# Optimization experiments

Hardware: AMD Instinct MI355X
Metric: run time of the kernel (lower is better)

## Reference

```python
import jax, jax.numpy as jnp
import numpy as np

BN_INV = 1.0 / np.float32(np.sqrt(1.0 + 1e-5))  # eval BN with running_mean=0, running_var=1


def _conv(x, w, stride):
    return jax.lax.conv_general_dilated(
        x, w, (stride, stride), [(1, 1), (1, 1)],
        dimension_numbers=('NCHW', 'OIHW', 'NCHW'))


def _se(x, w1, b1, w2, b2):
    # squeeze-excite: global avg pool -> fc -> relu -> fc -> sigmoid -> scale
    y = x.mean(axis=(2, 3))                       # (B, C)
    y = jax.nn.relu(y @ w1.T + b1)
    y = jax.nn.sigmoid(y @ w2.T + b2)
    return x * y[:, :, None, None]


def _squash(s):
    n2 = jnp.sum(s * s, axis=-1, keepdims=True)
    n = jnp.sqrt(n2)
    return s * (n2 / (1.0 + n2)) / (n + 1e-8)


def _block(x, cw, g, b, s1w, s1b, s2w, s2b, stride):
    h = _conv(x, cw, stride)
    h = h * (g * BN_INV)[None, :, None, None] + b[None, :, None, None]
    h = jax.nn.relu(h)
    return _se(h, s1w, s1b, s2w, s2b)


def setup_inputs() -> dict:
    key = jax.random.key(0)
    ks = jax.random.split(key, 32)
    rn = lambda i, shape, s=1.0: s * jax.random.normal(ks[i], shape, dtype=jnp.float32)
    d = {}
    d['x'] = rn(0, (64, 1, 128, 128))
    # feature extractor
    d['conv1_w'] = rn(1, (16, 1, 3, 3), 0.3)
    d['bn1_g'] = 1.0 + rn(2, (16,), 0.1)
    d['bn1_b'] = rn(3, (16,), 0.1)
    d['se1_w1'] = rn(4, (1, 16), 0.2); d['se1_b1'] = rn(5, (1,), 0.1)
    d['se1_w2'] = rn(6, (16, 1), 0.2); d['se1_b2'] = rn(7, (16,), 0.1)
    d['conv2_w'] = rn(8, (32, 16, 3, 3), 0.1)
    d['bn2_g'] = 1.0 + rn(9, (32,), 0.1)
    d['bn2_b'] = rn(10, (32,), 0.1)
    d['se2_w1'] = rn(11, (2, 32), 0.2); d['se2_b1'] = rn(12, (2,), 0.1)
    d['se2_w2'] = rn(13, (32, 2), 0.2); d['se2_b2'] = rn(14, (32,), 0.1)
    d['conv3_w'] = rn(15, (64, 32, 3, 3), 0.07)
    d['bn3_g'] = 1.0 + rn(16, (64,), 0.1)
    d['bn3_b'] = rn(17, (64,), 0.1)
    d['se3_w1'] = rn(18, (4, 64), 0.15); d['se3_b1'] = rn(19, (4,), 0.1)
    d['se3_w2'] = rn(20, (64, 4), 0.15); d['se3_b2'] = rn(21, (64,), 0.1)
    # primary capsules conv: 64 -> 8 caps * 8 dim = 64 channels, stride 2
    d['pc_w'] = rn(22, (64, 64, 3, 3), 0.05)
    d['pc_b'] = rn(23, (64,), 0.05)
    # digit capsule transform: (1, 2048, 3, 16, 8)
    d['W_digit'] = 0.01 * jax.random.normal(ks[24], (1, 2048, 3, 16, 8), dtype=jnp.float32)
    return d


def reference(x, conv1_w, bn1_g, bn1_b, se1_w1, se1_b1, se1_w2, se1_b2,
              conv2_w, bn2_g, bn2_b, se2_w1, se2_b1, se2_w2, se2_b2,
              conv3_w, bn3_g, bn3_b, se3_w1, se3_b1, se3_w2, se3_b2,
              pc_w, pc_b, W_digit):
    h = _block(x, conv1_w, bn1_g, bn1_b, se1_w1, se1_b1, se1_w2, se1_b2, 1)
    h = _block(h, conv2_w, bn2_g, bn2_b, se2_w1, se2_b1, se2_w2, se2_b2, 2)
    h = _block(h, conv3_w, bn3_g, bn3_b, se3_w1, se3_b1, se3_w2, se3_b2, 2)
    # primary capsules: conv -> (B, 8 caps, 8 dim, 16*16) -> (B, 2048, 8)
    u = _conv(h, pc_w, 2) + pc_b[None, :, None, None]     # (B, 64, 16, 16)
    B = u.shape[0]
    u = u.reshape(B, 8, 8, -1).transpose(0, 1, 3, 2).reshape(B, -1, 8)
    u = _squash(u)                                        # (B, 2048, 8)
    # u_hat[b,i,c,d] = sum_e W[0,i,c,d,e] * u[b,i,e]  (avoids torch's W.repeat)
    u_hat = jnp.einsum('icde,bie->bicd', W_digit[0], u)   # (B, 2048, 3, 16)
    b_ij = jnp.zeros((B, u_hat.shape[1], u_hat.shape[2], 1), u_hat.dtype)
    v_j = None
    for _ in range(3):  # fixed routing iterations
        c_ij = jax.nn.softmax(b_ij, axis=2)
        s_j = jnp.sum(c_ij * u_hat, axis=1, keepdims=True)  # (B,1,3,16)
        v_j = _squash(s_j)
        b_ij = b_ij + jnp.sum(u_hat * v_j, axis=-1, keepdims=True)
    v = v_j[:, 0]                                          # (B, 3, 16)
    return jnp.sqrt(jnp.sum(v * v, axis=-1))               # (B, 3) class lengths
```

## Files before the change

### kernel.cpp

```cpp
#include <hip/hip_runtime.h>
#include <math.h>

#define BN_INV_F 0.9999950000374997f

__device__ __forceinline__ void gload_lds4(const float* g, float* l) {
    __builtin_amdgcn_global_load_lds(
        (const __attribute__((address_space(1))) void*)g,
        (__attribute__((address_space(3))) void*)l, 4, 0, 0);
}
__device__ __forceinline__ void gload_lds16(const float* g, float* l) {
    __builtin_amdgcn_global_load_lds(
        (const __attribute__((address_space(1))) void*)g,
        (__attribute__((address_space(3))) void*)l, 16, 0, 0);
}

__global__ __launch_bounds__(256) void wtrans_all_k(
    const float* __restrict__ w1, const float* __restrict__ w2,
    const float* __restrict__ w3, const float* __restrict__ wp,
    float* __restrict__ w1t, float* __restrict__ w2t,
    float* __restrict__ w3t, float* __restrict__ wpt)
{
    int i = blockIdx.x * 256 + threadIdx.x;
    if (i < 144) {
        int co = i % 16, k = i / 16;
        w1t[i] = w1[co * 9 + k];
    } else if (i < 4752) {
        int t = i - 144;
        int co = t % 32, rk = t / 32, cin = rk / 9, k = rk % 9;
        w2t[t] = w2[(co * 16 + cin) * 9 + k];
    } else if (i < 23184) {
        int t = i - 4752;
        int co = t % 64, rk = t / 64, cin = rk / 9, k = rk % 9;
        w3t[t] = w3[(co * 32 + cin) * 9 + k];
    } else if (i < 60048) {
        int t = i - 23184;
        int co = t % 64, rk = t / 64, cin = rk / 9, k = rk % 9;
        wpt[t] = wp[(co * 64 + cin) * 9 + k];
    }
}

template <int CIN, int CINB, int COUT, int COB, int HIN, int HOUT, int STRIDE,
          int TW, int ROWS_T, int PPT, int CB, int NTHREADS,
          bool BN_RELU, bool SE_SUM, int HSE_IN, int KSPLIT>
__device__ __forceinline__ void conv_body(
    const float* __restrict__ in, const float* __restrict__ wt,
    const float* __restrict__ gamma, const float* __restrict__ beta,
    float* __restrict__ out, size_t pstride,
    float* __restrict__ se_sum, const float* __restrict__ se_sums_in,
    const float* __restrict__ se_w1, const float* __restrict__ se_b1,
    const float* __restrict__ se_w2, const float* __restrict__ se_b2,
    float inv_spatial)
{
    constexpr int WIN = HIN, WOUT = HOUT;
    constexpr int TH = ROWS_T * PPT;
    constexpr int IH_T = (TH - 1) * STRIDE + 3;
    constexpr int NW = NTHREADS / 64;
    constexpr int NCHUNK = CINB / CB;
    constexpr int SEGS = (WIN >= 64) ? (WIN / 64) : 1;
    constexpr int PAIRS = (IH_T + 1) / 2;
    constexpr int NG = COUT / COB;
    constexpr int IHW = IH_T * WIN;
    constexpr int CHUNK_BYTES = CB * IHW * 4;
    constexpr bool FAST16 = (CHUNK_BYTES % 1024) == 0;
    constexpr int NISS = CHUNK_BYTES / 1024;
    static_assert(NTHREADS == TW * ROWS_T, "geometry");
    static_assert(TW == WOUT, "tile must span full output width");
    static_assert(CINB % CB == 0, "chunking");
    static_assert(WIN % 64 == 0 || WIN == 32, "stage width");

    const int b = blockIdx.z;
    const int gy = blockIdx.y;
    const int ty = blockIdx.x;
    const int tid = threadIdx.x;
    const int wo = tid % TW;
    const int rg = tid / TW;
    const int g = gy % NG;
    const int kk = gy / NG;
    const int cin0 = kk * CINB;

    __shared__ float in_t[2][CB * IH_T * WIN];
    __shared__ float scl[CIN];
    __shared__ float gl[COB], bl[COB];
    __shared__ float red[NW][COB];
    __shared__ float hid[HSE_IN > 0 ? HSE_IN : 1];

    const float* inb = in + (size_t)b * CIN * HIN * WIN;
    const int gr0 = ty * TH * STRIDE - 1;
    const int wos = wo * STRIDE;
    const int wvid = tid >> 6, lane = tid & 63;
    const bool interior = (gr0 >= 0) && (gr0 + IH_T <= HIN);

    auto stage = [&](int c, int buf) {
        const int cb0 = cin0 + c * CB;
        float* bb = &in_t[buf][0];
        if (FAST16 && interior) {
            for (int i = wvid; i < NISS; i += NW) {
                int fe = i * 256 + lane * 4;
                int ci = fe / IHW;
                int rem = fe - ci * IHW;
                int lr = rem / WIN;
                int lc = rem - lr * WIN;
                const float* gsrc = inb + (size_t)(cb0 + ci) * (HIN * WIN)
                                  + (size_t)(gr0 + lr) * WIN + lc;
                gload_lds16(gsrc, bb + i * 256);
            }
        } else if (WIN >= 64) {
            for (int r = wvid; r < CB * IH_T; r += NW) {
                int ci = r / IH_T, lr = r - ci * IH_T;
                int gr = gr0 + lr;
                float* ldst = bb + (ci * IH_T + lr) * WIN;
                if (gr >= 0 && gr < HIN) {
                    const float* gsrc = inb + (size_t)(cb0 + ci) * HIN * WIN + (size_t)gr * WIN;
#pragma unroll
                    for (int s = 0; s < SEGS; ++s)
                        gload_lds4(gsrc + s * 64 + lane, ldst + s * 64);
                } else {
#pragma unroll
                    for (int s = 0; s < SEGS; ++s) ldst[s * 64 + lane] = 0.0f;
                }
            }
        } else {
            for (int pz = wvid; pz < CB * PAIRS; pz += NW) {
                int ci = pz / PAIRS, q = pz - ci * PAIRS;
                int lr0 = q * 2;
                int nr = (lr0 + 1 < IH_T) ? 2 : 1;
                int grr = gr0 + lr0;
                float* ldst = bb + (ci * IH_T + lr0) * WIN;
                if (nr == 2 && grr >= 0 && grr + 1 < HIN) {
                    const float* gsrc = inb + (size_t)(cb0 + ci) * HIN * WIN + (size_t)grr * WIN + lane;
                    gload_lds4(gsrc, ldst);
                } else {
                    for (int e = lane; e < nr * WIN; e += 64) {
                        int rr = e / WIN, cc = e - rr * WIN;
                        int gr = grr + rr;
                        ldst[e] = (gr >= 0 && gr < HIN)
                            ? inb[(size_t)(cb0 + ci) * HIN * WIN + (size_t)gr * WIN + cc] : 0.0f;
                    }
                }
            }
        }
    };

    stage(0, 0);

    if (HSE_IN > 0) {
        if (tid < HSE_IN) {
            float a = se_b1[tid];
            for (int c = 0; c < CIN; ++c)
                a = fmaf(se_sums_in[b * CIN + c] * inv_spatial, se_w1[tid * CIN + c], a);
            hid[tid] = fmaxf(a, 0.0f);
        }
        __syncthreads();
        if (tid < CIN) {
            float a = se_b2[tid];
            for (int h = 0; h < HSE_IN; ++h)
                a = fmaf(hid[h], se_w2[tid * HSE_IN + h], a);
            scl[tid] = 1.0f / (1.0f + expf(-a));
        }
    } else {
        for (int t = tid; t < CIN; t += NTHREADS) scl[t] = 1.0f;
    }
    if (tid < COB) {
        int co = g * COB + tid;
        if (BN_RELU) {
            gl[tid] = gamma[co] * BN_INV_F;
            bl[tid] = beta[co];
        } else {
            gl[tid] = (kk == 0) ? gamma[co] : 0.0f;
        }
    }

    float acc[PPT][COB];
#pragma unroll
    for (int p = 0; p < PPT; ++p)
#pragma unroll
        for (int co = 0; co < COB; ++co) acc[p][co] = 0.0f;

    int cur = 0;
    for (int c = 0; c < NCHUNK; ++c) {
        asm volatile("s_waitcnt vmcnt(0)" ::: "memory");
        __syncthreads();
        if (c + 1 < NCHUNK) stage(c + 1, cur ^ 1);

        const float* bb = &in_t[cur][0];
#pragma unroll
        for (int ci = 0; ci < CB; ++ci) {
            const int cw = cin0 + c * CB + ci;
            const float sc = scl[cw];
            const float* wtap = wt + (size_t)cw * 9 * COUT + g * COB;
            const float* bb_ci = bb + ci * IH_T * WIN;
#pragma unroll
            for (int kh = 0; kh < 3; ++kh) {
#pragma unroll
                for (int kw = 0; kw < 3; ++kw) {
                    const float* wrow = wtap + (kh * 3 + kw) * COUT;
#pragma unroll
                    for (int p = 0; p < PPT; ++p) {
                        const float* row = bb_ci + ((rg + p * ROWS_T) * STRIDE + kh) * WIN;
                        int wi = wos + kw - 1;
                        float v;
                        if (kw == 0) {
                            v = row[wi < 0 ? 0 : wi];
                            if (wi < 0) v = 0.0f;
                        } else if (STRIDE == 1 && kw == 2) {
                            v = row[wi >= WIN ? WIN - 1 : wi];
                            if (wi >= WIN) v = 0.0f;
                        } else {
                            v = row[wi];
                        }
                        v *= sc;
#pragma unroll
                        for (int co = 0; co < COB; ++co)
                            acc[p][co] = fmaf(wrow[co], v, acc[p][co]);
                    }
                }
            }
        }
        cur ^= 1;
    }

    float tsum[COB];
#pragma unroll
    for (int co = 0; co < COB; ++co) tsum[co] = 0.0f;
    float* ob = out + (size_t)kk * pstride
              + ((size_t)b * COUT + (size_t)g * COB) * HOUT * WOUT;
#pragma unroll
    for (int p = 0; p < PPT; ++p) {
        const int ho = ty * TH + rg + p * ROWS_T;
#pragma unroll
        for (int co = 0; co < COB; ++co) {
            float v;
            if (BN_RELU)
                v = fmaxf(fmaf(acc[p][co], gl[co], bl[co]), 0.0f);
            else
                v = acc[p][co] + gl[co];
            ob[(size_t)co * HOUT * WOUT + ho * WOUT + wo] = v;
            tsum[co] += v;
        }
    }

    if (SE_SUM) {
#pragma unroll
        for (int co = 0; co < COB; ++co) {
            float v = tsum[co];
            for (int off = 32; off; off >>= 1) v += __shfl_down(v, off, 64);
            if (lane == 0) red[wvid][co] = v;
        }
        __syncthreads();
        if (tid < COB) {
            float v = 0.0f;
#pragma unroll
            for (int k = 0; k < NW; ++k) v += red[k][tid];
            atomicAdd(&se_sum[b * COUT + g * COB + tid], v);
        }
    }
}

template <int CIN, int CINB, int COUT, int WCO, int HIN, int HOUT,
          int TW, int CB, int NTHREADS,
          bool BN_RELU, bool SE_SUM, int HSE_IN>
__device__ __forceinline__ void conv_ws2_body(
    const float* __restrict__ in, const float* __restrict__ wt,
    const float* __restrict__ gamma, const float* __restrict__ beta,
    float* __restrict__ out,
    float* __restrict__ se_sum, const float* __restrict__ se_sums_in,
    const float* __restrict__ se_w1, const float* __restrict__ se_b1,
    const float* __restrict__ se_w2, const float* __restrict__ se_b2,
    float inv_spatial)
{
    constexpr int WIN = HIN, WOUT = HOUT;
    constexpr int STRIDE = 2;
    constexpr int NW = NTHREADS / 64;
    constexpr int NP = TW / 2;
    constexpr int TH = 64 / NP;
    constexpr int IH_T = (TH - 1) * STRIDE + 3;
    constexpr int COBT = NW * WCO;
    constexpr int NG = COUT / COBT;
    constexpr int NCHUNK = CINB / CB;
    constexpr int SEGS = WIN / 64;
    constexpr int HALF = WIN / 2;
    constexpr int ROWS = CB * IH_T;
    constexpr int NPW = (ROWS / NW) * SEGS;
    static_assert(TW == WOUT, "tile spans full width");
    static_assert(CINB % CB == 0, "chunking");
    static_assert(WIN % 64 == 0, "stage width");
    static_assert(COUT % COBT == 0, "cout split");
    static_assert(ROWS % NW == 0, "uniform DMA count per wave");
    static_assert(NCHUNK >= 2, "pipeline depth");

    const int b = blockIdx.z;
    const int gy = blockIdx.y;
    const int ty = blockIdx.x;
    const int tid = threadIdx.x;
    const int lane = tid & 63;
    const int wvu = __builtin_amdgcn_readfirstlane(tid >> 6);
    const int wo2 = lane % NP;
    const int rl = lane / NP;
    const int g = gy % NG;
    const int kk = gy / NG;
    const int cin0 = kk * CINB;

    __shared__ float in_t[3][CB * IH_T * WIN];
    __shared__ float scl[CIN];
    __shared__ float gl[COBT], bl[COBT];
    __shared__ float red[NW][WCO];
    __shared__ float hid[HSE_IN > 0 ? HSE_IN : 1];

    const float* inb = in + (size_t)b * CIN * HIN * WIN;
    const int gr0 = ty * TH * STRIDE - 1;
    const bool interior = (gr0 >= 0) && (gr0 + IH_T <= HIN);

    auto stage = [&](int c, int buf) {
        const int cb0 = cin0 + c * CB;
        float* bb = &in_t[buf][0];
        if (interior) {
            for (int r = wvu; r < ROWS; r += NW) {
                int ci = r / IH_T, lr = r - ci * IH_T;
                const float* gsrc = inb + (size_t)(cb0 + ci) * HIN * WIN + (size_t)(gr0 + lr) * WIN;
                float* ldst = bb + r * WIN;
#pragma unroll
                for (int s = 0; s < SEGS; ++s) {
                    int p = s * 64 + lane;
                    int half = p / HALF;
                    int idx = p - half * HALF;
                    gload_lds4(gsrc + 2 * idx + half, ldst + s * 64);
                }
            }
        } else {
            for (int r = wvu; r < ROWS; r += NW) {
                int ci = r / IH_T, lr = r - ci * IH_T;
                int gr = gr0 + lr;
                float* ldst = bb + r * WIN;
                if (gr >= 0 && gr < HIN) {
                    const float* gsrc = inb + (size_t)(cb0 + ci) * HIN * WIN + (size_t)gr * WIN;
#pragma unroll
                    for (int s = 0; s < SEGS; ++s) {
                        int p = s * 64 + lane;
                        int half = p / HALF;
                        int idx = p - half * HALF;
                        gload_lds4(gsrc + 2 * idx + half, ldst + s * 64);
                    }
                } else {
#pragma unroll
                    for (int s = 0; s < SEGS; ++s) ldst[s * 64 + lane] = 0.0f;
                }
            }
        }
    };

    if (HSE_IN > 0) {
        if (tid < HSE_IN) {
            float a = se_b1[tid];
            for (int c = 0; c < CIN; ++c)
                a = fmaf(se_sums_in[b * CIN + c] * inv_spatial, se_w1[tid * CIN + c], a);
            hid[tid] = fmaxf(a, 0.0f);
        }
        __syncthreads();
        if (tid < CIN) {
            float a = se_b2[tid];
            for (int h = 0; h < HSE_IN; ++h)
                a = fmaf(hid[h], se_w2[tid * HSE_IN + h], a);
            scl[tid] = 1.0f / (1.0f + expf(-a));
        }
    } else {
        for (int t = tid; t < CIN; t += NTHREADS) scl[t] = 1.0f;
    }
    if (tid < COBT) {
        int co = g * COBT + tid;
        if (BN_RELU) {
            gl[tid] = gamma[co] * BN_INV_F;
            bl[tid] = beta[co];
        } else {
            gl[tid] = (kk == 0) ? gamma[co] : 0.0f;
        }
    }
    __syncthreads();

    stage(0, 0);
    stage(1, 1);

    float acc0[WCO], acc1[WCO];
#pragma unroll
    for (int co = 0; co < WCO; ++co) { acc0[co] = 0.0f; acc1[co] = 0.0f; }

    for (int c = 0; c < NCHUNK; ++c) {
        if (interior) {
            if (c + 1 < NCHUNK)
                asm volatile("s_waitcnt vmcnt(%0)" :: "i"(NPW) : "memory");
            else
                asm volatile("s_waitcnt vmcnt(0)" ::: "memory");
        } else {
            asm volatile("s_waitcnt vmcnt(0) lgkmcnt(0)" ::: "memory");
        }
        __builtin_amdgcn_s_barrier();
        __builtin_amdgcn_sched_barrier(0);
        if (c + 2 < NCHUNK) stage(c + 2, (c + 2) % 3);

        const float* bb = &in_t[c % 3][0];
#pragma unroll
        for (int ci = 0; ci < CB; ++ci) {
            const int cw = cin0 + c * CB + ci;
            const float sc = scl[cw];
            const float* wtap = wt + (size_t)cw * 9 * COUT + g * COBT + wvu * WCO;
            const float* bb_ci = bb + ci * IH_T * WIN;
#pragma unroll
            for (int kh = 0; kh < 3; ++kh) {
                const float* row = bb_ci + (rl * STRIDE + kh) * WIN;
                float2 E2 = *(const float2*)(row + 2 * wo2);
                float2 O2 = *(const float2*)(row + HALF + 2 * wo2);
                float om = __shfl_up(O2.y, 1, 64);
                if (wo2 == 0) om = 0.0f;
                const float vm0 = om   * sc;
                const float ve0 = E2.x * sc;
                const float vp0 = O2.x * sc;
                const float ve1 = E2.y * sc;
                const float vp1 = O2.y * sc;
                const float* w0 = wtap + (kh * 3 + 0) * COUT;
                const float* w1 = wtap + (kh * 3 + 1) * COUT;
                const float* w2 = wtap + (kh * 3 + 2) * COUT;
#pragma unroll
                for (int co = 0; co < WCO; ++co) {
                    acc0[co] = fmaf(w0[co], vm0, acc0[co]);
                    acc0[co] = fmaf(w1[co], ve0, acc0[co]);
                    acc0[co] = fmaf(w2[co], vp0, acc0[co]);
                    acc1[co] = fmaf(w0[co], vp0, acc1[co]);
                    acc1[co] = fmaf(w1[co], ve1, acc1[co]);
                    acc1[co] = fmaf(w2[co], vp1, acc1[co]);
                }
            }
        }
    }

    float tsum[WCO];
#pragma unroll
    for (int co = 0; co < WCO; ++co) tsum[co] = 0.0f;
    const int ho = ty * TH + rl;
    float* ob = out + ((size_t)b * COUT + (size_t)g * COBT + (size_t)wvu * WCO) * HOUT * WOUT;
#pragma unroll
    for (int co = 0; co < WCO; ++co) {
        float v0, v1;
        const float gg = gl[wvu * WCO + co];
        if (BN_RELU) {
            const float bb2 = bl[wvu * WCO + co];
            v0 = fmaxf(fmaf(acc0[co], gg, bb2), 0.0f);
            v1 = fmaxf(fmaf(acc1[co], gg, bb2), 0.0f);
        } else {
            v0 = acc0[co] + gg;
            v1 = acc1[co] + gg;
        }
        float2 vv; vv.x = v0; vv.y = v1;
        *(float2*)(ob + (size_t)co * HOUT * WOUT + (size_t)ho * WOUT + 2 * wo2) = vv;
        tsum[co] += v0 + v1;
    }

    if (SE_SUM) {
#pragma unroll
        for (int co = 0; co < WCO; ++co) {
            float v = tsum[co];
            for (int off = 32; off; off >>= 1) v += __shfl_down(v, off, 64);
            if (lane == 0) red[wvu][co] = v;
        }
        __syncthreads();
        if (lane < WCO)
            atomicAdd(&se_sum[b * COUT + g * COBT + wvu * WCO + lane], red[wvu][lane]);
    }
}

#define CONV_ARGS \
    const float* __restrict__ in, const float* __restrict__ wt, \
    const float* __restrict__ gamma, const float* __restrict__ beta, \
    float* __restrict__ out, size_t pstride, float* __restrict__ se_sum, \
    const float* __restrict__ se_sums_in, \
    const float* __restrict__ se_w1, const float* __restrict__ se_b1, \
    const float* __restrict__ se_w2, const float* __restrict__ se_b2, \
    float inv_spatial
#define CONV_PASS in, wt, gamma, beta, out, pstride, se_sum, se_sums_in, \
    se_w1, se_b1, se_w2, se_b2, inv_spatial
#define CONV_PASS2 in, wt, gamma, beta, out, se_sum, se_sums_in, \
    se_w1, se_b1, se_w2, se_b2, inv_spatial

__global__ __launch_bounds__(256) void conv1_k(CONV_ARGS) {
    conv_body<1, 1, 16, 16, 128, 128, 1, 128, 2, 2, 1, 256, true, true, 0, 1>(CONV_PASS);
}
__global__ __launch_bounds__(256) void conv2_k(CONV_ARGS) {
    conv_ws2_body<16, 16, 32, 8, 128, 64, 64, 4, 256, true, true, 1>(CONV_PASS2);
}
__global__ __launch_bounds__(256) void conv3_k(CONV_ARGS) {
    conv_ws2_body<32, 32, 64, 8, 64, 32, 32, 4, 256, true, true, 2>(CONV_PASS2);
}
__global__ __launch_bounds__(256) void pc_k(CONV_ARGS) {
    conv_body<64, 16, 64, 16, 32, 16, 2, 16, 16, 1, 4, 256, false, false, 4, 4>(CONV_PASS);
}

__global__ __launch_bounds__(256) void squash_uhat_k(
    const float* __restrict__ up, size_t pstride,
    const float* __restrict__ W, float* __restrict__ u_hat)
{
    const int base = blockIdx.x * 256;
    const int tid = threadIdx.x;
    __shared__ float ush[256][8];

    {
        const int cap = base + tid;
        const int b = cap >> 11, i = cap & 2047;
        const int chi = i >> 8, spx = i & 255;
        const size_t off = ((size_t)(b * 64 + chi * 8)) * 256 + spx;
        float s[8];
        float n2 = 0.0f;
#pragma unroll
        for (int j = 0; j < 8; j++) {
            const size_t o = off + (size_t)j * 256;
            s[j] = (up[o] + up[o + pstride]) + (up[o + 2 * pstride] + up[o + 3 * pstride]);
            n2 = fmaf(s[j], s[j], n2);
        }
        const float n = sqrtf(n2);
        const float f = (n2 / (1.0f + n2)) / (n + 1e-8f);
#pragma unroll
        for (int j = 0; j < 8; j++) ush[tid][j] = s[j] * f;
    }
    __syncthreads();

    float* ob = u_hat + (size_t)base * 48;
#pragma unroll 4
    for (int k = 0; k < 48; ++k) {
        int o = tid + k * 256;
        int c = o / 48, cd = o % 48;
        int gi = (base + c) & 2047;
        const float* wp = W + (size_t)gi * 384 + cd * 8;
        float a = 0.0f;
#pragma unroll
        for (int e = 0; e < 8; e++) a = fmaf(wp[e], ush[c][e], a);
        ob[o] = a;
    }
}

template <int IT>
__global__ __launch_bounds__(256) void sweep_k(const float* __restrict__ u_hat,
                                               const float* __restrict__ s_hist,
                                               float* __restrict__ s_out)
{
    const int b = blockIdx.y;
    const int i = blockIdx.x * 256 + threadIdx.x;
    const int tid = threadIdx.x;
    __shared__ float vsh[IT > 0 ? IT : 1][48];
    __shared__ float fac[IT > 0 ? IT : 1][3];
    __shared__ float red[4][48];

    const float4* qp = (const float4*)(u_hat + ((size_t)b * 2048 + i) * 48);
    float uhv[48];
#pragma unroll
    for (int q = 0; q < 12; ++q) {
        float4 t = qp[q];
        uhv[q * 4 + 0] = t.x; uhv[q * 4 + 1] = t.y;
        uhv[q * 4 + 2] = t.z; uhv[q * 4 + 3] = t.w;
    }

    if (IT > 0) {
        if (tid < IT * 48) {
            int t = tid / 48, c = tid % 48;
            vsh[t][c] = s_hist[((size_t)t * 64 + b) * 48 + c];
        }
        __syncthreads();
        if (tid < IT * 3) {
            int t = tid / 3, j = tid % 3;
            float n2 = 0.0f;
            for (int d = 0; d < 16; ++d) { float s = vsh[t][j * 16 + d]; n2 = fmaf(s, s, n2); }
            float n = sqrtf(n2);
            fac[t][j] = (n2 / (1.0f + n2)) / (n + 1e-8f);
        }
        __syncthreads();
        if (tid < IT * 48) {
            int t = tid / 48, c = tid % 48;
            vsh[t][c] *= fac[t][c / 16];
        }
        __syncthreads();
    }

    float c0, c1, c2;
    if (IT == 0) {
        c0 = c1 = c2 = (1.0f / 3.0f);
    } else {
        float b0 = 0.0f, b1 = 0.0f, b2 = 0.0f;
#pragma unroll
        for (int t = 0; t < IT; ++t)
#pragma unroll
            for (int d = 0; d < 16; ++d) {
                b0 = fmaf(uhv[d],      vsh[t][d],      b0);
                b1 = fmaf(uhv[16 + d], vsh[t][16 + d], b1);
                b2 = fmaf(uhv[32 + d], vsh[t][32 + d], b2);
            }
        float m = fmaxf(b0, fmaxf(b1, b2));
        float e0 = expf(b0 - m), e1 = expf(b1 - m), e2 = expf(b2 - m);
        float inv = 1.0f / (e0 + e1 + e2);
        c0 = e0 * inv; c1 = e1 * inv; c2 = e2 * inv;
    }

    float sp[48];
#pragma unroll
    for (int d = 0; d < 16; ++d) {
        sp[d]      = c0 * uhv[d];
        sp[16 + d] = c1 * uhv[16 + d];
        sp[32 + d] = c2 * uhv[32 + d];
    }
    const int lane = tid & 63, wv = tid >> 6;
#pragma unroll
    for (int j = 0; j < 48; ++j) {
        float x = sp[j];
        for (int off = 32; off; off >>= 1) x += __shfl_down(x, off, 64);
        if (lane == 0) red[wv][j] = x;
    }
    __syncthreads();
    if (tid < 48) {
        float x = red[0][tid] + red[1][tid] + red[2][tid] + red[3][tid];
        atomicAdd(&s_out[(size_t)b * 48 + tid], x);
    }
}

__global__ __launch_bounds__(64) void route_out_k(const float* __restrict__ s2,
                                                  float* __restrict__ out)
{
    const int b = blockIdx.x;
    __shared__ float s[48];
    if (threadIdx.x < 48) s[threadIdx.x] = s2[(size_t)b * 48 + threadIdx.x];
    __syncthreads();
    if (threadIdx.x < 3) {
        int j = threadIdx.x;
        float n2 = 0.0f;
        for (int d = 0; d < 16; ++d) { float v = s[j * 16 + d]; n2 = fmaf(v, v, n2); }
        float n = sqrtf(n2);
        float fc = (n2 / (1.0f + n2)) / (n + 1e-8f);
        out[b * 3 + j] = fc * n;
    }
}

extern "C" void kernel_launch(void* const* d_in, const int* in_sizes, int n_in,
                              void* d_out, int out_size, void* d_ws, size_t ws_size,
                              hipStream_t stream)
{
    const float* x       = (const float*)d_in[0];
    const float* conv1_w = (const float*)d_in[1];
    const float* bn1_g   = (const float*)d_in[2];
    const float* bn1_b   = (const float*)d_in[3];
    const float* se1_w1  = (const float*)d_in[4];
    const float* se1_b1  = (const float*)d_in[5];
    const float* se1_w2  = (const float*)d_in[6];
    const float* se1_b2  = (const float*)d_in[7];
    const float* conv2_w = (const float*)d_in[8];
    const float* bn2_g   = (const float*)d_in[9];
    const float* bn2_b   = (const float*)d_in[10];
    const float* se2_w1  = (const float*)d_in[11];
    const float* se2_b1  = (const float*)d_in[12];
    const float* se2_w2  = (const float*)d_in[13];
    const float* se2_b2  = (const float*)d_in[14];
    const float* conv3_w = (const float*)d_in[15];
    const float* bn3_g   = (const float*)d_in[16];
    const float* bn3_b   = (const float*)d_in[17];
    const float* se3_w1  = (const float*)d_in[18];
    const float* se3_b1  = (const float*)d_in[19];
    const float* se3_w2  = (const float*)d_in[20];
    const float* se3_b2  = (const float*)d_in[21];
    const float* pc_w    = (const float*)d_in[22];
    const float* pc_b    = (const float*)d_in[23];
    const float* W_digit = (const float*)d_in[24];

    float* ws = (float*)d_ws;
    float* h1     = ws;
    float* h2     = ws + 16777216;
    float* h3     = ws;
    float* uparts = ws + 4194304;
    float* u_hat  = ws + 9437184;
    float* sums   = ws + 25165824;
    float* s1 = sums, *s2 = sums + 1024, *s3 = sums + 3072;
    float* s_buf  = sums + 7168;
    float* w1t    = ws + 25182272;
    float* w2t    = w1t + 144;
    float* w3t    = w2t + 4608;
    float* wpt    = w3t + 18432;

    hipMemsetAsync(sums, 0, 16448 * sizeof(float), stream);
    wtrans_all_k<<<235, 256, 0, stream>>>(conv1_w, conv2_w, conv3_w, pc_w,
                                          w1t, w2t, w3t, wpt);

    conv1_k<<<dim3(32, 1, 64), 256, 0, stream>>>(
        x, w1t, bn1_g, bn1_b, h1, 0, s1,
        nullptr, nullptr, nullptr, nullptr, nullptr, 0.0f);

    conv2_k<<<dim3(32, 1, 64), 256, 0, stream>>>(
        h1, w2t, bn2_g, bn2_b, h2, 0, s2,
        s1, se1_w1, se1_b1, se1_w2, se1_b2, 1.0f / 16384.0f);

    conv3_k<<<dim3(8, 2, 64), 256, 0, stream>>>(
        h2, w3t, bn3_g, bn3_b, h3, 0, s3,
        s2, se2_w1, se2_b1, se2_w2, se2_b2, 1.0f / 4096.0f);

    pc_k<<<dim3(1, 16, 64), 256, 0, stream>>>(
        h3, wpt, pc_b, nullptr, uparts, (size_t)1048576, nullptr,
        s3, se3_w1, se3_b1, se3_w2, se3_b2, 1.0f / 1024.0f);

    squash_uhat_k<<<512, 256, 0, stream>>>(uparts, (size_t)1048576, W_digit, u_hat);

    sweep_k<0><<<dim3(8, 64), 256, 0, stream>>>(u_hat, s_buf, s_buf + 0 * 64 * 48);
    sweep_k<1><<<dim3(8, 64), 256, 0, stream>>>(u_hat, s_buf, s_buf + 1 * 64 * 48);
    sweep_k<2><<<dim3(8, 64), 256, 0, stream>>>(u_hat, s_buf, s_buf + 2 * 64 * 48);
    route_out_k<<<64, 64, 0, stream>>>(s_buf + 2 * 64 * 48, (float*)d_out);
}
```

Before: 212.2 us.

## Switch stride-2 conv to double buffering with vector-register float4 weight loads

Replaces the triple-buffered LDS pipeline, which used fine-grained vmcnt waits, with a simpler double buffer that waits for all loads and issues a full barrier each chunk. The first stage now starts before the SE/BN prologue so it overlaps that work. Adding an opaque zero VGPR to the weight pointer makes it divergent, which moves the weight reads from scalar loads to per-lane float4 vector loads. This trades prefetch depth and more vector memory traffic for less LDS, and it relies on the WCO==8 layout.

```diff
diff --git a/kernel.cpp b/kernel.cpp
--- a/kernel.cpp
+++ b/kernel.cpp
@@ -280,12 +280,11 @@
     constexpr int SEGS = WIN / 64;
     constexpr int HALF = WIN / 2;
     constexpr int ROWS = CB * IH_T;
-    constexpr int NPW = (ROWS / NW) * SEGS;
+    static_assert(WCO == 8, "float4-pair weight loads assume WCO==8");
     static_assert(TW == WOUT, "tile spans full width");
     static_assert(CINB % CB == 0, "chunking");
     static_assert(WIN % 64 == 0, "stage width");
     static_assert(COUT % COBT == 0, "cout split");
-    static_assert(ROWS % NW == 0, "uniform DMA count per wave");
     static_assert(NCHUNK >= 2, "pipeline depth");
 
     const int b = blockIdx.z;
@@ -300,7 +299,10 @@
     const int kk = gy / NG;
     const int cin0 = kk * CINB;
 
-    __shared__ float in_t[3][CB * IH_T * WIN];
+    int vzero;
+    asm volatile("v_mov_b32 %0, 0" : "=v"(vzero));
+
+    __shared__ float in_t[2][CB * IH_T * WIN];
     __shared__ float scl[CIN];
     __shared__ float gl[COBT], bl[COBT];
     __shared__ float red[NW][WCO];
@@ -348,6 +350,8 @@
         }
     };
 
+    stage(0, 0);
+
     if (HSE_IN > 0) {
         if (tid < HSE_IN) {
             float a = se_b1[tid];
@@ -374,34 +378,23 @@
             gl[tid] = (kk == 0) ? gamma[co] : 0.0f;
         }
     }
-    __syncthreads();
-
-    stage(0, 0);
-    stage(1, 1);
 
     float acc0[WCO], acc1[WCO];
 #pragma unroll
     for (int co = 0; co < WCO; ++co) { acc0[co] = 0.0f; acc1[co] = 0.0f; }
 
+    int cur = 0;
     for (int c = 0; c < NCHUNK; ++c) {
-        if (interior) {
-            if (c + 1 < NCHUNK)
-                asm volatile("s_waitcnt vmcnt(%0)" :: "i"(NPW) : "memory");
-            else
-                asm volatile("s_waitcnt vmcnt(0)" ::: "memory");
-        } else {
-            asm volatile("s_waitcnt vmcnt(0) lgkmcnt(0)" ::: "memory");
-        }
-        __builtin_amdgcn_s_barrier();
-        __builtin_amdgcn_sched_barrier(0);
-        if (c + 2 < NCHUNK) stage(c + 2, (c + 2) % 3);
-
-        const float* bb = &in_t[c % 3][0];
+        asm volatile("s_waitcnt vmcnt(0)" ::: "memory");
+        __syncthreads();
+        if (c + 1 < NCHUNK) stage(c + 1, cur ^ 1);
+
+        const float* bb = &in_t[cur][0];
 #pragma unroll
         for (int ci = 0; ci < CB; ++ci) {
             const int cw = cin0 + c * CB + ci;
             const float sc = scl[cw];
-            const float* wtap = wt + (size_t)cw * 9 * COUT + g * COBT + wvu * WCO;
+            const float* wtap = wt + (size_t)cw * 9 * COUT + g * COBT + wvu * WCO + vzero;
             const float* bb_ci = bb + ci * IH_T * WIN;
 #pragma unroll
             for (int kh = 0; kh < 3; ++kh) {
@@ -415,20 +408,27 @@
                 const float vp0 = O2.x * sc;
                 const float ve1 = E2.y * sc;
                 const float vp1 = O2.y * sc;
-                const float* w0 = wtap + (kh * 3 + 0) * COUT;
-                const float* w1 = wtap + (kh * 3 + 1) * COUT;
-                const float* w2 = wtap + (kh * 3 + 2) * COUT;
+                const float4* q0 = (const float4*)(wtap + (kh * 3 + 0) * COUT);
+                const float4* q1 = (const float4*)(wtap + (kh * 3 + 1) * COUT);
+                const float4* q2 = (const float4*)(wtap + (kh * 3 + 2) * COUT);
+                float4 w0a = q0[0], w0b = q0[1];
+                float4 w1a = q1[0], w1b = q1[1];
+                float4 w2a = q2[0], w2b = q2[1];
+                float w0v[8] = {w0a.x, w0a.y, w0a.z, w0a.w, w0b.x, w0b.y, w0b.z, w0b.w};
+                float w1v[8] = {w1a.x, w1a.y, w1a.z, w1a.w, w1b.x, w1b.y, w1b.z, w1b.w};
+                float w2v[8] = {w2a.x, w2a.y, w2a.z, w2a.w, w2b.x, w2b.y, w2b.z, w2b.w};
 #pragma unroll
                 for (int co = 0; co < WCO; ++co) {
-                    acc0[co] = fmaf(w0[co], vm0, acc0[co]);
-                    acc0[co] = fmaf(w1[co], ve0, acc0[co]);
-                    acc0[co] = fmaf(w2[co], vp0, acc0[co]);
-                    acc1[co] = fmaf(w0[co], vp0, acc1[co]);
-                    acc1[co] = fmaf(w1[co], ve1, acc1[co]);
-                    acc1[co] = fmaf(w2[co], vp1, acc1[co]);
+                    acc0[co] = fmaf(w0v[co], vm0, acc0[co]);
+                    acc0[co] = fmaf(w1v[co], ve0, acc0[co]);
+                    acc0[co] = fmaf(w2v[co], vp0, acc0[co]);
+                    acc1[co] = fmaf(w0v[co], vp0, acc1[co]);
+                    acc1[co] = fmaf(w1v[co], ve1, acc1[co]);
+                    acc1[co] = fmaf(w2v[co], vp1, acc1[co]);
                 }
             }
         }
+        cur ^= 1;
     }
 
     float tsum[WCO];
```

Result: slower. 287.3 us (+35.4%).
